# Optimization experiments

Hardware: AMD Instinct MI355X
Metric: run time of the kernel (lower is better)

## Reference

```python
import jax, jax.numpy as jnp
import numpy as np

MAX_STEP = 20

def setup_inputs() -> dict:
    key = jax.random.key(0)
    k1, k2 = jax.random.split(key)
    B, L, E, H = 32, 2048, 256, 256
    word_rep = jax.random.normal(k1, (B, L, E), dtype=jnp.float32)
    # nn.Parameter(torch.randn(...).uniform_(-0.1, 0.1)) -> uniform in [-0.1, 0.1]
    cnn = jax.random.uniform(k2, (MAX_STEP, E, H), dtype=jnp.float32, minval=-0.1, maxval=0.1)
    return {"word_rep": word_rep, "cnn": cnn}

def reference(word_rep, cnn):
    # word_rep: [B, L, E]; cnn: [MAX_STEP, E, H]
    L = word_rep.shape[1]
    # Gather the cyclically-indexed per-position weight: [L, E, H]
    W = cnn[jnp.arange(L) % MAX_STEP]
    # Fused batched matmul over all positions at once: [B, L, H]
    hidden_vecs = jnp.einsum('ble,leh->blh', word_rep, W)
    return (hidden_vecs, hidden_vecs[:, -1])
```

## Files before the change

### kernel.cpp

```cpp
#include <hip/hip_runtime.h>
#include <hip/hip_bf16.h>

#define B_ 32
#define L_ 2048
#define E_ 256
#define H_ 256
#define MAXSTEP 20
#define NL 4
#define NCH 26
#define NGRP (MAXSTEP * NCH)

typedef __attribute__((ext_vector_type(4))) float f32x4;
typedef __attribute__((ext_vector_type(8))) short bf16x8;
using bf16 = __hip_bfloat16;

__device__ inline short cvt1(float x) {
    bf16 b = __float2bfloat16(x);
    return *reinterpret_cast<short*>(&b);
}

__global__ void transpose_w_kernel(const float* __restrict__ cnn, short* __restrict__ wt) {
    __shared__ short tile[32][33];
    const int s  = blockIdx.z;
    const int e0 = blockIdx.y * 32;
    const int h0 = blockIdx.x * 32;
    const int tx = threadIdx.x;
    const int ty = threadIdx.y;
    const float* src = cnn + ((size_t)s * E_ + e0) * H_ + h0;
#pragma unroll
    for (int i = ty; i < 32; i += 8)
        tile[i][tx] = cvt1(src[(size_t)i * H_ + tx]);
    __syncthreads();
    short* dst = wt + ((size_t)s * H_ + h0) * E_ + e0;
#pragma unroll
    for (int i = ty; i < 32; i += 8)
        dst[(size_t)i * E_ + tx] = tile[tx][i];
}

__global__ __launch_bounds__(256, 2) void vaw_swap_kernel(
        const float* __restrict__ A, const short* __restrict__ Wt,
        float* __restrict__ out) {
    __shared__ __align__(16) float aLds[2][B_ * E_];

    const int g_    = blockIdx.x;
    const int s     = g_ / NCH;
    const int chunk = g_ % NCH;
    const int cnt   = (s < 8) ? 103 : 102;
    const int wv    = threadIdx.x >> 6;
    const int lane  = threadIdx.x & 63;
    const int r     = lane & 15;
    const int g     = lane >> 4;
    const int nbase = wv * 64;
    const int key   = r & 7;

    const short* wtb = Wt + ((size_t)s * H_ + nbase + r) * E_ + g * 8;
    bf16x8 breg[8][4];
#pragma unroll
    for (int kk = 0; kk < 8; ++kk)
#pragma unroll
        for (int nf = 0; nf < 4; ++nf)
            breg[kk][nf] = *(const bf16x8*)(wtb + (size_t)nf * 16 * E_ + kk * 32);

    auto lof = [&](int il) {
        int idx = chunk * NL + il;
        if (idx > cnt - 1) idx = cnt - 1;
        return s + 20 * idx;
    };

    auto stage = [&](int it) {
        const int l = lof(it);
        float* dst = aLds[it & 1];
#pragma unroll
        for (int t = 0; t < 8; ++t) {
            const int b  = t * 4 + wv;
            const int cg = lane ^ (b & 7);
            const float* gp = A + ((size_t)b * L_ + l) * E_ + cg * 4;
            __builtin_amdgcn_global_load_lds(
                (const __attribute__((address_space(1))) void*)gp,
                (__attribute__((address_space(3))) void*)&dst[b * 256],
                16, 0, 0);
        }
    };

    stage(0);

#pragma unroll 1
    for (int it = 0; it < NL; ++it) {
        const int l   = lof(it);
        const int cur = it & 1;

        if (it < NL - 1) stage(it + 1);

        if (it == 0)          asm volatile("s_waitcnt vmcnt(8)"  ::: "memory");
        else if (it < NL - 1) asm volatile("s_waitcnt vmcnt(16)" ::: "memory");
        else                  asm volatile("s_waitcnt vmcnt(8)"  ::: "memory");
        __builtin_amdgcn_s_barrier();
        __builtin_amdgcn_sched_barrier(0);

        f32x4 acc[4][2];
#pragma unroll
        for (int nf = 0; nf < 4; ++nf)
#pragma unroll
            for (int hf = 0; hf < 2; ++hf)
                acc[nf][hf] = f32x4{0.f, 0.f, 0.f, 0.f};

#pragma unroll
        for (int kk = 0; kk < 8; ++kk) {
            const int c0 = kk * 8 + g * 2;
            f32x4 a0lo = *(const f32x4*)&aLds[cur][r * 256 + ((c0 ^ key) << 2)];
            f32x4 a0hi = *(const f32x4*)&aLds[cur][r * 256 + (((c0 + 1) ^ key) << 2)];
            f32x4 a1lo = *(const f32x4*)&aLds[cur][(r + 16) * 256 + ((c0 ^ key) << 2)];
            f32x4 a1hi = *(const f32x4*)&aLds[cur][(r + 16) * 256 + (((c0 + 1) ^ key) << 2)];
            bf16x8 a0, a1;
#pragma unroll
            for (int j = 0; j < 4; ++j) {
                a0[j]     = cvt1(a0lo[j]);
                a0[j + 4] = cvt1(a0hi[j]);
                a1[j]     = cvt1(a1lo[j]);
                a1[j + 4] = cvt1(a1hi[j]);
            }
#pragma unroll
            for (int nf = 0; nf < 4; ++nf) {
                acc[nf][0] = __builtin_amdgcn_mfma_f32_16x16x32_bf16(breg[kk][nf], a0, acc[nf][0], 0, 0, 0);
                acc[nf][1] = __builtin_amdgcn_mfma_f32_16x16x32_bf16(breg[kk][nf], a1, acc[nf][1], 0, 0, 0);
            }
        }

#pragma unroll
        for (int hf = 0; hf < 2; ++hf) {
            const int b = r + 16 * hf;
            float* orow = out + ((size_t)b * L_ + l) * H_ + nbase + g * 4;
#pragma unroll
            for (int nf = 0; nf < 4; ++nf)
                *(f32x4*)(orow + nf * 16) = acc[nf][hf];
        }
        if (l == L_ - 1) {
            float* out2 = out + (size_t)B_ * L_ * H_;
#pragma unroll
            for (int hf = 0; hf < 2; ++hf) {
                const int b = r + 16 * hf;
                float* orow = out2 + (size_t)b * H_ + nbase + g * 4;
#pragma unroll
                for (int nf = 0; nf < 4; ++nf)
                    *(f32x4*)(orow + nf * 16) = acc[nf][hf];
            }
        }

        __builtin_amdgcn_s_barrier();
    }
}

__global__ __launch_bounds__(256) void vaw_fallback_kernel(
        const float* __restrict__ A, const float* __restrict__ W, float* __restrict__ out) {
    __shared__ __align__(16) float aLds[2][B_ * E_];
    const int l0   = blockIdx.x * 4;
    const int wv   = threadIdx.x >> 6;
    const int lane = threadIdx.x & 63;
    const int r    = lane & 15;
    const int g    = lane >> 4;
    const int nbase = wv * 64;
    const int key   = r & 7;

    auto stage = [&](int it) {
        float* dst = aLds[it & 1];
        const int l = l0 + it;
#pragma unroll
        for (int t = 0; t < 8; ++t) {
            const int b  = t * 4 + wv;
            const int cgx = lane ^ (b & 7);
            const float* gp = A + ((size_t)b * L_ + l) * E_ + cgx * 4;
            __builtin_amdgcn_global_load_lds(
                (const __attribute__((address_space(1))) void*)gp,
                (__attribute__((address_space(3))) void*)&dst[b * 256],
                16, 0, 0);
        }
    };

    stage(0);
#pragma unroll 1
    for (int it = 0; it < 4; ++it) {
        const int l   = l0 + it;
        const int sidx = l % MAXSTEP;
        const int cur = it & 1;
        if (it < 3) {
            stage(it + 1);
            asm volatile("s_waitcnt vmcnt(8)" ::: "memory");
        } else {
            asm volatile("s_waitcnt vmcnt(0)" ::: "memory");
        }
        __builtin_amdgcn_s_barrier();
        __builtin_amdgcn_sched_barrier(0);

        f32x4 acc[2][4] = {};
        const float* Wf = W + (size_t)sidx * E_ * H_;
#pragma unroll 2
        for (int kk = 0; kk < 8; ++kk) {
            const int k0 = kk * 32;
            const int c0 = kk * 8 + g * 2;
            f32x4 a0lo = *(const f32x4*)&aLds[cur][r * 256 + ((c0 ^ key) << 2)];
            f32x4 a0hi = *(const f32x4*)&aLds[cur][r * 256 + (((c0 + 1) ^ key) << 2)];
            f32x4 a1lo = *(const f32x4*)&aLds[cur][(r + 16) * 256 + ((c0 ^ key) << 2)];
            f32x4 a1hi = *(const f32x4*)&aLds[cur][(r + 16) * 256 + (((c0 + 1) ^ key) << 2)];
            bf16x8 a0, a1;
#pragma unroll
            for (int j = 0; j < 4; ++j) {
                a0[j]     = cvt1(a0lo[j]);
                a0[j + 4] = cvt1(a0hi[j]);
                a1[j]     = cvt1(a1lo[j]);
                a1[j + 4] = cvt1(a1hi[j]);
            }
            bf16x8 b0, b1, b2, b3;
#pragma unroll
            for (int j = 0; j < 8; ++j) {
                const size_t krow = (size_t)(k0 + g * 8 + j) * H_;
                b0[j] = cvt1(Wf[krow + nbase +  0 + r]);
                b1[j] = cvt1(Wf[krow + nbase + 16 + r]);
                b2[j] = cvt1(Wf[krow + nbase + 32 + r]);
                b3[j] = cvt1(Wf[krow + nbase + 48 + r]);
            }
            acc[0][0] = __builtin_amdgcn_mfma_f32_16x16x32_bf16(a0, b0, acc[0][0], 0, 0, 0);
            acc[0][1] = __builtin_amdgcn_mfma_f32_16x16x32_bf16(a0, b1, acc[0][1], 0, 0, 0);
            acc[0][2] = __builtin_amdgcn_mfma_f32_16x16x32_bf16(a0, b2, acc[0][2], 0, 0, 0);
            acc[0][3] = __builtin_amdgcn_mfma_f32_16x16x32_bf16(a0, b3, acc[0][3], 0, 0, 0);
            acc[1][0] = __builtin_amdgcn_mfma_f32_16x16x32_bf16(a1, b0, acc[1][0], 0, 0, 0);
            acc[1][1] = __builtin_amdgcn_mfma_f32_16x16x32_bf16(a1, b1, acc[1][1], 0, 0, 0);
            acc[1][2] = __builtin_amdgcn_mfma_f32_16x16x32_bf16(a1, b2, acc[1][2], 0, 0, 0);
            acc[1][3] = __builtin_amdgcn_mfma_f32_16x16x32_bf16(a1, b3, acc[1][3], 0, 0, 0);
        }

        const int row0 = g * 4;
#pragma unroll
        for (int mf = 0; mf < 2; ++mf)
#pragma unroll
            for (int nf = 0; nf < 4; ++nf) {
                const int h = nbase + nf * 16 + r;
#pragma unroll
                for (int i = 0; i < 4; ++i) {
                    const int bb = mf * 16 + row0 + i;
                    out[((size_t)bb * L_ + l) * H_ + h] = acc[mf][nf][i];
                }
            }
        if (l == L_ - 1) {
            float* out2 = out + (size_t)B_ * L_ * H_;
#pragma unroll
            for (int mf = 0; mf < 2; ++mf)
#pragma unroll
                for (int nf = 0; nf < 4; ++nf) {
                    const int h = nbase + nf * 16 + r;
#pragma unroll
                    for (int i = 0; i < 4; ++i) {
                        const int bb = mf * 16 + row0 + i;
                        out2[(size_t)bb * H_ + h] = acc[mf][nf][i];
                    }
                }
        }
        __builtin_amdgcn_s_barrier();
    }
}

extern "C" void kernel_launch(void* const* d_in, const int* in_sizes, int n_in,
                              void* d_out, int out_size, void* d_ws, size_t ws_size,
                              hipStream_t stream) {
    const float* word_rep = (const float*)d_in[0];
    const float* cnn      = (const float*)d_in[1];
    float* out = (float*)d_out;

    const size_t wt_bytes = (size_t)MAXSTEP * E_ * H_ * sizeof(short);
    if (ws_size >= wt_bytes) {
        short* wt = (short*)d_ws;
        transpose_w_kernel<<<dim3(8, 8, 20), dim3(32, 8), 0, stream>>>(cnn, wt);
        vaw_swap_kernel<<<dim3(NGRP), dim3(256), 0, stream>>>(word_rep, wt, out);
    } else {
        vaw_fallback_kernel<<<dim3(L_ / 4), dim3(256), 0, stream>>>(word_rep, cnn, out);
    }
}
```

Before: 46.72 us.

## Pre-convert activations to bf16 in workspace and use a bf16-staged MFMA kernel

Adds a separate pass that converts word_rep to bf16 in the workspace. A new GEMM kernel then stages the bf16 activations directly into LDS in MFMA fragment layout, so the in-loop fp32-to-bf16 conversion and swizzled loads go away. LDS use is halved, and the grid doubles because each block now handles two positions instead of four. The cost is an extra full read of the fp32 input plus a bf16 write, which adds memory traffic and another kernel launch.

```diff
diff --git a/kernel.cpp b/kernel.cpp
--- a/kernel.cpp
+++ b/kernel.cpp
@@ -6,9 +6,9 @@
 #define E_ 256
 #define H_ 256
 #define MAXSTEP 20
-#define NL 4
-#define NCH 26
-#define NGRP (MAXSTEP * NCH)
+#define NL 2
+#define NCH2 52
+#define NGRP2 (MAXSTEP * NCH2)
 
 typedef __attribute__((ext_vector_type(4))) float f32x4;
 typedef __attribute__((ext_vector_type(8))) short bf16x8;
@@ -17,6 +17,22 @@
 __device__ inline short cvt1(float x) {
     bf16 b = __float2bfloat16(x);
     return *reinterpret_cast<short*>(&b);
+}
+
+__global__ __launch_bounds__(256) void convert_a_kernel(
+        const float* __restrict__ A, short* __restrict__ Abf, int n8) {
+    for (int i = blockIdx.x * blockDim.x + threadIdx.x; i < n8; i += gridDim.x * blockDim.x) {
+        const float* p = A + (size_t)i * 8;
+        f32x4 lo = *(const f32x4*)p;
+        f32x4 hi = *(const f32x4*)(p + 4);
+        bf16x8 v;
+#pragma unroll
+        for (int j = 0; j < 4; ++j) {
+            v[j]     = cvt1(lo[j]);
+            v[j + 4] = cvt1(hi[j]);
+        }
+        *(bf16x8*)(Abf + (size_t)i * 8) = v;
+    }
 }
 
 __global__ void transpose_w_kernel(const float* __restrict__ cnn, short* __restrict__ wt) {
@@ -37,11 +53,117 @@
         dst[(size_t)i * E_ + tx] = tile[tx][i];
 }
 
+__global__ __launch_bounds__(256, 2) void vaw_bf16_kernel(
+        const short* __restrict__ Abf, const short* __restrict__ Wt,
+        float* __restrict__ out) {
+    __shared__ __align__(16) short aLds[2][8192];
+
+    const int g_    = blockIdx.x;
+    const int s     = g_ / NCH2;
+    const int chunk = g_ % NCH2;
+    const int cnt   = (s < 8) ? 103 : 102;
+    const int wv    = threadIdx.x >> 6;
+    const int lane  = threadIdx.x & 63;
+    const int r     = lane & 15;
+    const int g     = lane >> 4;
+    const int nbase = wv * 64;
+
+    const short* wtb = Wt + ((size_t)s * H_ + nbase + r) * E_ + g * 8;
+    bf16x8 breg[8][4];
+#pragma unroll
+    for (int kk = 0; kk < 8; ++kk)
+#pragma unroll
+        for (int nf = 0; nf < 4; ++nf)
+            breg[kk][nf] = *(const bf16x8*)(wtb + (size_t)nf * 16 * E_ + kk * 32);
+    __builtin_amdgcn_sched_barrier(0);
+
+    auto lof = [&](int il) {
+        int idx = chunk * NL + il;
+        if (idx > cnt - 1) idx = cnt - 1;
+        return s + 20 * idx;
+    };
+
+    const int rl = lane >> 2;
+    const int gc = lane & 3;
+    auto stage = [&](int it) {
+        const int l = lof(it);
+        short* dst = aLds[it & 1];
+#pragma unroll
+        for (int j = 0; j < 4; ++j) {
+            const int idx  = wv * 4 + j;
+            const int kk   = idx >> 1;
+            const int half = idx & 1;
+            const int b    = half * 16 + rl;
+            const short* gp = Abf + ((size_t)b * L_ + l) * E_ + kk * 32 + gc * 8;
+            __builtin_amdgcn_global_load_lds(
+                (const __attribute__((address_space(1))) void*)gp,
+                (__attribute__((address_space(3))) void*)&dst[idx * 512],
+                16, 0, 0);
+        }
+    };
+
+    stage(0);
+    stage(1);
+    __builtin_amdgcn_sched_barrier(0);
+
+#pragma unroll
+    for (int it = 0; it < NL; ++it) {
+        const int l   = lof(it);
+        const int cur = it & 1;
+
+        if (it == 0) asm volatile("s_waitcnt vmcnt(4)" ::: "memory");
+        else         asm volatile("s_waitcnt vmcnt(8)" ::: "memory");
+        __builtin_amdgcn_s_barrier();
+        __builtin_amdgcn_sched_barrier(0);
+
+        f32x4 acc[4][2];
+#pragma unroll
+        for (int nf = 0; nf < 4; ++nf)
+#pragma unroll
+            for (int hf = 0; hf < 2; ++hf)
+                acc[nf][hf] = f32x4{0.f, 0.f, 0.f, 0.f};
+
+#pragma unroll
+        for (int kk = 0; kk < 8; ++kk) {
+            bf16x8 a0 = *(const bf16x8*)&aLds[cur][kk * 1024 + (r * 4 + g) * 8];
+            bf16x8 a1 = *(const bf16x8*)&aLds[cur][kk * 1024 + 512 + (r * 4 + g) * 8];
+#pragma unroll
+            for (int nf = 0; nf < 4; ++nf) {
+                acc[nf][0] = __builtin_amdgcn_mfma_f32_16x16x32_bf16(breg[kk][nf], a0, acc[nf][0], 0, 0, 0);
+                acc[nf][1] = __builtin_amdgcn_mfma_f32_16x16x32_bf16(breg[kk][nf], a1, acc[nf][1], 0, 0, 0);
+            }
+        }
+
+#pragma unroll
+        for (int hf = 0; hf < 2; ++hf) {
+            const int b = r + 16 * hf;
+            float* orow = out + ((size_t)b * L_ + l) * H_ + nbase + g * 4;
+#pragma unroll
+            for (int nf = 0; nf < 4; ++nf)
+                *(f32x4*)(orow + nf * 16) = acc[nf][hf];
+        }
+        if (l == L_ - 1) {
+            float* out2 = out + (size_t)B_ * L_ * H_;
+#pragma unroll
+            for (int hf = 0; hf < 2; ++hf) {
+                const int b = r + 16 * hf;
+                float* orow = out2 + (size_t)b * H_ + nbase + g * 4;
+#pragma unroll
+                for (int nf = 0; nf < 4; ++nf)
+                    *(f32x4*)(orow + nf * 16) = acc[nf][hf];
+            }
+        }
+
+        __builtin_amdgcn_s_barrier();
+    }
+}
+
+#define NCH 26
+#define NGRP (MAXSTEP * NCH)
 __global__ __launch_bounds__(256, 2) void vaw_swap_kernel(
         const float* __restrict__ A, const short* __restrict__ Wt,
         float* __restrict__ out) {
     __shared__ __align__(16) float aLds[2][B_ * E_];
-
     const int g_    = blockIdx.x;
     const int s     = g_ / NCH;
     const int chunk = g_ % NCH;
@@ -62,11 +184,10 @@
             breg[kk][nf] = *(const bf16x8*)(wtb + (size_t)nf * 16 * E_ + kk * 32);
 
     auto lof = [&](int il) {
-        int idx = chunk * NL + il;
+        int idx = chunk * 4 + il;
         if (idx > cnt - 1) idx = cnt - 1;
         return s + 20 * idx;
     };
-
     auto stage = [&](int it) {
         const int l = lof(it);
         float* dst = aLds[it & 1];
@@ -83,17 +204,14 @@
     };
 
     stage(0);
-
 #pragma unroll 1
-    for (int it = 0; it < NL; ++it) {
+    for (int it = 0; it < 4; ++it) {
         const int l   = lof(it);
         const int cur = it & 1;
-
-        if (it < NL - 1) stage(it + 1);
-
-        if (it == 0)          asm volatile("s_waitcnt vmcnt(8)"  ::: "memory");
-        else if (it < NL - 1) asm volatile("s_waitcnt vmcnt(16)" ::: "memory");
-        else                  asm volatile("s_waitcnt vmcnt(8)"  ::: "memory");
+        if (it < 3) stage(it + 1);
+        if (it == 0)      asm volatile("s_waitcnt vmcnt(8)"  ::: "memory");
+        else if (it < 3)  asm volatile("s_waitcnt vmcnt(16)" ::: "memory");
+        else              asm volatile("s_waitcnt vmcnt(8)"  ::: "memory");
         __builtin_amdgcn_s_barrier();
         __builtin_amdgcn_sched_barrier(0);
 
@@ -145,7 +263,6 @@
                     *(f32x4*)(orow + nf * 16) = acc[nf][hf];
             }
         }
-
         __builtin_amdgcn_s_barrier();
     }
 }
@@ -265,8 +382,17 @@
     const float* cnn      = (const float*)d_in[1];
     float* out = (float*)d_out;
 
-    const size_t wt_bytes = (size_t)MAXSTEP * E_ * H_ * sizeof(short);
-    if (ws_size >= wt_bytes) {
+    const size_t wt_bytes  = (size_t)MAXSTEP * E_ * H_ * sizeof(short);
+    const size_t abf_bytes = (size_t)B_ * L_ * E_ * sizeof(short);
+
+    if (ws_size >= wt_bytes + abf_bytes) {
+        short* wt  = (short*)d_ws;
+        short* abf = (short*)((char*)d_ws + wt_bytes);
+        transpose_w_kernel<<<dim3(8, 8, 20), dim3(32, 8), 0, stream>>>(cnn, wt);
+        const int n8 = B_ * L_ * E_ / 8;
+        convert_a_kernel<<<dim3(2048), dim3(256), 0, stream>>>(word_rep, abf, n8);
+        vaw_bf16_kernel<<<dim3(NGRP2), dim3(256), 0, stream>>>(abf, wt, out);
+    } else if (ws_size >= wt_bytes) {
         short* wt = (short*)d_ws;
         transpose_w_kernel<<<dim3(8, 8, 20), dim3(32, 8), 0, stream>>>(cnn, wt);
         vaw_swap_kernel<<<dim3(NGRP), dim3(256), 0, stream>>>(word_rep, wt, out);
```

New measurement: 60.99 us. 1.31x slower.
